# Optimization experiments

Measured on AMD Instinct MI355X. Metric: run time of the kernel, lower is better.

## Reference

```python
import jax, jax.numpy as jnp
import numpy as np

NEG_SLOPE = 0.2  # leaky_relu negative slope (alpha)

def _glorot(key, shape):
    fan_in, fan_out = shape[0], shape[-1]
    lim = jnp.sqrt(6.0 / (fan_in + fan_out))
    return jax.random.uniform(key, shape, jnp.float32, -lim, lim)

def setup_inputs() -> dict:
    key = jax.random.key(0)
    ks = jax.random.split(key, 10)
    N, E, F_IN, HID, HEADS, NCLASS = 50000, 800000, 512, 32, 8, 32
    x = jax.random.normal(ks[0], (N, F_IN), jnp.float32)
    edge_index = jax.random.randint(ks[1], (2, E), 0, N, jnp.int64)
    # layer 1: heads=8, out per head = 32, concat -> 256
    W1 = _glorot(ks[2], (F_IN, HEADS * HID))
    att_src1 = _glorot(ks[3], (HEADS, HID))
    att_dst1 = _glorot(ks[4], (HEADS, HID))
    b1 = jnp.zeros((HEADS * HID,), jnp.float32)
    # layer 2: heads=1, out = nclass
    W2 = _glorot(ks[5], (HEADS * HID, NCLASS))
    att_src2 = _glorot(ks[6], (1, NCLASS))
    att_dst2 = _glorot(ks[7], (1, NCLASS))
    b2 = jnp.zeros((NCLASS,), jnp.float32)
    return {"x": x, "edge_index": edge_index, "W1": W1, "att_src1": att_src1,
            "att_dst1": att_dst1, "b1": b1, "W2": W2, "att_src2": att_src2,
            "att_dst2": att_dst2, "b2": b2}

def gat_conv(x, src, dst, W, a_src, a_dst, bias, num_nodes):
    """PyG GATConv (eval mode, self loops already appended to src/dst)."""
    H, C = a_src.shape
    h = (x @ W).reshape(num_nodes, H, C)                 # [N,H,C]
    score_src = jnp.einsum('nhc,hc->nh', h, a_src)       # [N,H]
    score_dst = jnp.einsum('nhc,hc->nh', h, a_dst)       # [N,H]
    e = jax.nn.leaky_relu(score_src[src] + score_dst[dst], NEG_SLOPE)  # [E,H]
    m = jax.ops.segment_max(e, dst, num_segments=num_nodes)           # [N,H]
    w = jnp.exp(e - m[dst])
    denom = jax.ops.segment_sum(w, dst, num_segments=num_nodes)       # [N,H]
    alpha = w / (denom[dst] + 1e-16)                                  # [E,H]
    out = jax.ops.segment_sum(alpha[:, :, None] * h[src], dst,
                              num_segments=num_nodes)                 # [N,H,C]
    return out.reshape(num_nodes, H * C) + bias

def reference(x, edge_index, W1, att_src1, att_dst1, b1, W2, att_src2, att_dst2, b2):
    N = x.shape[0]
    loops = jnp.arange(N, dtype=edge_index.dtype)
    src = jnp.concatenate([edge_index[0], loops])  # PyG add_self_loops=True
    dst = jnp.concatenate([edge_index[1], loops])
    h = jax.nn.elu(gat_conv(x, src, dst, W1, att_src1, att_dst1, b1, N))
    out = gat_conv(h, src, dst, W2, att_src2, att_dst2, b2, N)
    return out + 1e-06
```

## Files before the change

### kernel.cpp

```cpp
#include <hip/hip_runtime.h>
#include <math.h>

#define N_NODES 50000
#define N_EDGES 800000
#define E2 (N_EDGES + N_NODES)
#define F_IN 512
#define HEADS 8
#define HID 32
#define HC 256
#define NCLASS 32
#define NEG_SLOPE 0.2f

typedef unsigned int uint;
typedef unsigned short ushort;
typedef __attribute__((ext_vector_type(8))) short bf16x8;
typedef __attribute__((ext_vector_type(4))) float f32x4;

#define GLOBAL_LOAD_LDS16(g, l) \
    __builtin_amdgcn_global_load_lds((const __attribute__((address_space(1))) void*)(g), \
                                     (__attribute__((address_space(3))) void*)(l), 16, 0, 0)

__device__ inline uint bf16_rne_bits(float f) {
    uint u = __float_as_uint(f);
    return (u + 0x7fffu + ((u >> 16) & 1u)) >> 16;
}
__device__ inline float bf2f(ushort u) { return __uint_as_float(((uint)u) << 16); }

__global__ void split_w1t_kernel(const float* __restrict__ W1,
                                 ushort* __restrict__ hi, ushort* __restrict__ lo) {
    int t = blockIdx.x * 256 + threadIdx.x;
    int n = t >> 9, k = t & 511;
    float f = W1[k * 256 + n];
    uint h = bf16_rne_bits(f);
    float r = f - __uint_as_float(h << 16);
    hi[t] = (ushort)h;
    lo[t] = (ushort)bf16_rne_bits(r);
}

__global__ void split_w2t_kernel(const float* __restrict__ W2,
                                 ushort* __restrict__ hi, ushort* __restrict__ lo) {
    int t = blockIdx.x * 256 + threadIdx.x;
    int n = t >> 8, k = t & 255;
    float f = W2[k * 32 + n];
    uint h = bf16_rne_bits(f);
    float r = f - __uint_as_float(h << 16);
    hi[t] = (ushort)h;
    lo[t] = (ushort)bf16_rne_bits(r);
}

__global__ void __launch_bounds__(256) gemm1_mfma_kernel(const uint* __restrict__ xp,
        const ushort* __restrict__ bhi, const ushort* __restrict__ blo,
        const float* __restrict__ as1, const float* __restrict__ ad1,
        ushort* __restrict__ C, float* __restrict__ ssrc, float* __restrict__ sdst, int M) {
    __shared__ uint   As[128 * 32];
    __shared__ ushort Bh[128 * 32];
    __shared__ ushort Bl[128 * 32];
    const int tid = threadIdx.x, lane = tid & 63, wave = tid >> 6;
    const int bm = blockIdx.x * 128, bn = blockIdx.y * 128;

    const uint* agp[4]; const uint* alp[4];
    #pragma unroll
    for (int s = 0; s < 4; ++s) {
        int t = wave * 4 + s;
        int p = t * 64 + lane;
        int row = p >> 3, cs = p & 7;
        int c = cs ^ (row & 7);
        int grow = bm + row; if (grow > M - 1) grow = M - 1;
        agp[s] = xp + ((size_t)grow * 512 + c * 4);
        alp[s] = &As[t * 256];
    }
    const ushort* bhgp[2]; const ushort* blgp[2]; const ushort* bhlp[2]; const ushort* bllp[2];
    #pragma unroll
    for (int s = 0; s < 2; ++s) {
        int t = wave * 2 + s;
        int p = t * 64 + lane;
        int row = p >> 2, qs = p & 3;
        int q = qs ^ ((row >> 1) & 3);
        size_t go = (size_t)(bn + row) * 512 + q * 8;
        bhgp[s] = bhi + go; blgp[s] = blo + go;
        bhlp[s] = &Bh[t * 512]; bllp[s] = &Bl[t * 512];
    }

    f32x4 acc[4][4] = {};
    const int wm = (wave >> 1) * 64, wn = (wave & 1) * 64;
    const int fm = lane & 15, quad = lane >> 4;

    for (int kk = 0; kk < 16; ++kk) {
        #pragma unroll
        for (int s = 0; s < 4; ++s) GLOBAL_LOAD_LDS16(agp[s], alp[s]);
        #pragma unroll
        for (int s = 0; s < 2; ++s) {
            GLOBAL_LOAD_LDS16(bhgp[s], bhlp[s]);
            GLOBAL_LOAD_LDS16(blgp[s], bllp[s]);
        }
        #pragma unroll
        for (int s = 0; s < 4; ++s) agp[s] += 32;
        #pragma unroll
        for (int s = 0; s < 2; ++s) { bhgp[s] += 32; blgp[s] += 32; }
        __syncthreads();

        bf16x8 ah[4], al[4], bh[4], bl[4];
        #pragma unroll
        for (int i = 0; i < 4; ++i) {
            int row = wm + i * 16 + fm;
            int sw = row & 7;
            uint4 c0 = *(const uint4*)&As[row * 32 + (((2 * quad)     ^ sw) * 4)];
            uint4 c1 = *(const uint4*)&As[row * 32 + (((2 * quad + 1) ^ sw) * 4)];
            union { uint u[4]; bf16x8 v; } H, L;
            H.u[0] = __builtin_amdgcn_perm(c0.y, c0.x, 0x07060302u);
            H.u[1] = __builtin_amdgcn_perm(c0.w, c0.z, 0x07060302u);
            H.u[2] = __builtin_amdgcn_perm(c1.y, c1.x, 0x07060302u);
            H.u[3] = __builtin_amdgcn_perm(c1.w, c1.z, 0x07060302u);
            uint r0 = __float_as_uint(__uint_as_float(c0.x) - __uint_as_float(c0.x & 0xffff0000u));
            uint r1 = __float_as_uint(__uint_as_float(c0.y) - __uint_as_float(c0.y & 0xffff0000u));
            uint r2 = __float_as_uint(__uint_as_float(c0.z) - __uint_as_float(c0.z & 0xffff0000u));
            uint r3 = __float_as_uint(__uint_as_float(c0.w) - __uint_as_float(c0.w & 0xffff0000u));
            uint r4 = __float_as_uint(__uint_as_float(c1.x) - __uint_as_float(c1.x & 0xffff0000u));
            uint r5 = __float_as_uint(__uint_as_float(c1.y) - __uint_as_float(c1.y & 0xffff0000u));
            uint r6 = __float_as_uint(__uint_as_float(c1.z) - __uint_as_float(c1.z & 0xffff0000u));
            uint r7 = __float_as_uint(__uint_as_float(c1.w) - __uint_as_float(c1.w & 0xffff0000u));
            L.u[0] = __builtin_amdgcn_perm(r1, r0, 0x07060302u);
            L.u[1] = __builtin_amdgcn_perm(r3, r2, 0x07060302u);
            L.u[2] = __builtin_amdgcn_perm(r5, r4, 0x07060302u);
            L.u[3] = __builtin_amdgcn_perm(r7, r6, 0x07060302u);
            ah[i] = H.v; al[i] = L.v;
        }
        #pragma unroll
        for (int j = 0; j < 4; ++j) {
            int row = wn + j * 16 + fm;
            int qs = quad ^ ((row >> 1) & 3);
            bh[j] = *(const bf16x8*)&Bh[row * 32 + qs * 8];
            bl[j] = *(const bf16x8*)&Bl[row * 32 + qs * 8];
        }
        #pragma unroll
        for (int i = 0; i < 4; ++i)
            #pragma unroll
            for (int j = 0; j < 4; ++j) {
                acc[i][j] = __builtin_amdgcn_mfma_f32_16x16x32_bf16(ah[i], bh[j], acc[i][j], 0, 0, 0);
                acc[i][j] = __builtin_amdgcn_mfma_f32_16x16x32_bf16(ah[i], bl[j], acc[i][j], 0, 0, 0);
                acc[i][j] = __builtin_amdgcn_mfma_f32_16x16x32_bf16(al[i], bh[j], acc[i][j], 0, 0, 0);
            }
        __syncthreads();
    }

    #pragma unroll
    for (int i = 0; i < 4; ++i) {
        int rb = bm + wm + i * 16 + quad * 4;
        #pragma unroll
        for (int j = 0; j < 4; ++j) {
            int col = bn + wn + j * 16 + fm;
            #pragma unroll
            for (int r = 0; r < 4; ++r) {
                int row = rb + r;
                if (row < M) C[(size_t)row * 256 + col] = (ushort)bf16_rne_bits(acc[i][j][r]);
            }
        }
    }

    const int head0 = (bn + wn) >> 5;
    const float asA0 = as1[head0 * 32 + fm],      asA1 = as1[head0 * 32 + 16 + fm];
    const float asB0 = as1[head0 * 32 + 32 + fm], asB1 = as1[head0 * 32 + 48 + fm];
    const float adA0 = ad1[head0 * 32 + fm],      adA1 = ad1[head0 * 32 + 16 + fm];
    const float adB0 = ad1[head0 * 32 + 32 + fm], adB1 = ad1[head0 * 32 + 48 + fm];
    #pragma unroll
    for (int i = 0; i < 4; ++i) {
        #pragma unroll
        for (int r = 0; r < 4; ++r) {
            int row = bm + wm + i * 16 + quad * 4 + r;
            float s1A = acc[i][0][r] * asA0 + acc[i][1][r] * asA1;
            float s1B = acc[i][2][r] * asB0 + acc[i][3][r] * asB1;
            float s2A = acc[i][0][r] * adA0 + acc[i][1][r] * adA1;
            float s2B = acc[i][2][r] * adB0 + acc[i][3][r] * adB1;
            #pragma unroll
            for (int off = 1; off < 16; off <<= 1) {
                s1A += __shfl_xor(s1A, off);
                s1B += __shfl_xor(s1B, off);
                s2A += __shfl_xor(s2A, off);
                s2B += __shfl_xor(s2B, off);
            }
            if (fm == 0 && row < M) {
                ssrc[(size_t)row * 8 + head0]     = s1A;
                ssrc[(size_t)row * 8 + head0 + 1] = s1B;
                sdst[(size_t)row * 8 + head0]     = s2A;
                sdst[(size_t)row * 8 + head0 + 1] = s2B;
            }
        }
    }
}

__global__ void __launch_bounds__(256) gemm2_mfma_kernel(const ushort* __restrict__ A,
        const ushort* __restrict__ bh_g, const ushort* __restrict__ bl_g,
        const float* __restrict__ as2, const float* __restrict__ ad2,
        ushort* __restrict__ C, float* __restrict__ ssrc, float* __restrict__ sdst, int M) {
    __shared__ ushort As[128 * 32];
    const int tid = threadIdx.x, lane = tid & 63, wave = tid >> 6;
    const int bm = blockIdx.x * 128;
    const int fm = lane & 15, quad = lane >> 4;
    const int wrow = wave * 32;

    const ushort* agp[2]; const ushort* alp[2];
    #pragma unroll
    for (int s = 0; s < 2; ++s) {
        int t = wave * 2 + s;
        int p = t * 64 + lane;
        int row = p >> 2, qs = p & 3;
        int q = qs ^ ((row >> 1) & 3);
        int gr = bm + row; if (gr > M - 1) gr = M - 1;
        agp[s] = A + (size_t)gr * 256 + q * 8;
        alp[s] = &As[t * 512];
    }

    f32x4 acc[2][2] = {};
    for (int kk = 0; kk < 8; ++kk) {
        GLOBAL_LOAD_LDS16(agp[0], alp[0]);
        GLOBAL_LOAD_LDS16(agp[1], alp[1]);
        agp[0] += 32; agp[1] += 32;
        __syncthreads();
        bf16x8 a[2], bh[2], bl[2];
        #pragma unroll
        for (int i = 0; i < 2; ++i) {
            int row = wrow + i * 16 + fm;
            int q = quad ^ ((row >> 1) & 3);
            a[i] = *(const bf16x8*)&As[row * 32 + q * 8];
        }
        #pragma unroll
        for (int j = 0; j < 2; ++j) {
            size_t off = (size_t)(j * 16 + fm) * 256 + kk * 32 + quad * 8;
            bh[j] = *(const bf16x8*)(bh_g + off);
            bl[j] = *(const bf16x8*)(bl_g + off);
        }
        #pragma unroll
        for (int i = 0; i < 2; ++i)
            #pragma unroll
            for (int j = 0; j < 2; ++j) {
                acc[i][j] = __builtin_amdgcn_mfma_f32_16x16x32_bf16(a[i], bh[j], acc[i][j], 0, 0, 0);
                acc[i][j] = __builtin_amdgcn_mfma_f32_16x16x32_bf16(a[i], bl[j], acc[i][j], 0, 0, 0);
            }
        __syncthreads();
    }

    float a0 = as2[fm], a1 = as2[16 + fm];
    float d0 = ad2[fm], d1 = ad2[16 + fm];
    #pragma unroll
    for (int i = 0; i < 2; ++i) {
        #pragma unroll
        for (int r = 0; r < 4; ++r) {
            int rg = bm + wrow + i * 16 + quad * 4 + r;
            float v0 = acc[i][0][r], v1 = acc[i][1][r];
            float s1 = v0 * a0 + v1 * a1;
            float s2 = v0 * d0 + v1 * d1;
            #pragma unroll
            for (int off = 1; off < 16; off <<= 1) {
                s1 += __shfl_xor(s1, off);
                s2 += __shfl_xor(s2, off);
            }
            if (rg < M) {
                C[(size_t)rg * 32 + fm]      = (ushort)bf16_rne_bits(v0);
                C[(size_t)rg * 32 + 16 + fm] = (ushort)bf16_rne_bits(v1);
                if (fm == 0) { ssrc[rg] = s1; sdst[rg] = s2; }
            }
        }
    }
}

__global__ void count_deg(const int* __restrict__ ei, int* __restrict__ deg) {
    int e = blockIdx.x * blockDim.x + threadIdx.x;
    if (e >= E2) return;
    int dst = (e < N_EDGES) ? ei[N_EDGES + e] : (e - N_EDGES);
    atomicAdd(&deg[dst], 1);
}

#define SCAN_B 256
#define SCAN_NB ((N_NODES + SCAN_B - 1) / SCAN_B)

__global__ void scan1_kernel(const int* __restrict__ deg, int* __restrict__ rowstart,
                             int* __restrict__ blocksum) {
    __shared__ int sm[SCAN_B];
    int t = threadIdx.x, i = blockIdx.x * SCAN_B + t;
    int v = (i < N_NODES) ? deg[i] : 0;
    sm[t] = v; __syncthreads();
    int x = v;
    for (int off = 1; off < SCAN_B; off <<= 1) {
        int y = (t >= off) ? sm[t - off] : 0; __syncthreads();
        x += y; sm[t] = x; __syncthreads();
    }
    if (i <= N_NODES) rowstart[i] = x - v;
    if (t == SCAN_B - 1) blocksum[blockIdx.x] = x;
}

__global__ void scan2_kernel(const int* __restrict__ blocksum, int* __restrict__ blockoff) {
    __shared__ int sm[256];
    int t = threadIdx.x;
    int v = (t < SCAN_NB) ? blocksum[t] : 0;
    sm[t] = v; __syncthreads();
    int x = v;
    for (int off = 1; off < 256; off <<= 1) {
        int y = (t >= off) ? sm[t - off] : 0; __syncthreads();
        x += y; sm[t] = x; __syncthreads();
    }
    if (t < SCAN_NB) blockoff[t] = x - v;
}

__global__ void fill_csr(const int* __restrict__ ei, const int* __restrict__ rowstart,
                         const int* __restrict__ blockoff,
                         int* __restrict__ cursor, int* __restrict__ csr_src) {
    int e = blockIdx.x * blockDim.x + threadIdx.x;
    if (e >= E2) return;
    int src, dst;
    if (e < N_EDGES) { src = ei[e]; dst = ei[N_EDGES + e]; }
    else             { src = e - N_EDGES; dst = src; }
    int p = atomicAdd(&cursor[dst], 1);
    csr_src[rowstart[dst] + blockoff[dst >> 8] + p] = src;
}

__global__ void __launch_bounds__(256) agg1_wave_kernel(const ushort* __restrict__ h,
        const float* __restrict__ ssrc, const float* __restrict__ sdst,
        const int* __restrict__ rowstart, const int* __restrict__ blockoff,
        const int* __restrict__ csr_src,
        const float* __restrict__ bias, ushort* __restrict__ out) {
    const int wid = (blockIdx.x * blockDim.x + threadIdx.x) >> 6;
    if (wid >= N_NODES) return;
    const int lane = threadIdx.x & 63;
    const int hg = lane >> 3;
    const int hl = lane & 7;
    const int n = wid;
    const int beg = rowstart[n] + blockoff[n >> 8];
    const int end = rowstart[n + 1] + blockoff[(n + 1) >> 8];
    const float sdst_n = sdst[(size_t)n * HEADS + hg];

    float4 acc = make_float4(0.f, 0.f, 0.f, 0.f);
    float sw = 0.f;
    const ushort* hc = h + lane * 4;
    const int base = hg << 3;
    for (int e = beg; e < end; e += 8) {
        int ee = e + hl;
        int eidx = ee < end ? ee : end - 1;
        int src_h = csr_src[eidx];
        float sc = ssrc[(size_t)src_h * HEADS + hg] + sdst_n;
        sc = sc > 0.f ? sc : NEG_SLOPE * sc;
        float w_h = (ee < end) ? __expf(sc) : 0.f;
        float wj[8]; int sj[8];
        #pragma unroll
        for (int j = 0; j < 8; ++j) {
            wj[j] = __shfl(w_h, base + j);
            sj[j] = __shfl(src_h, base + j);
        }
        ushort4 v[8];
        #pragma unroll
        for (int j = 0; j < 8; ++j) v[j] = *(const ushort4*)(hc + (size_t)sj[j] * HC);
        #pragma unroll
        for (int j = 0; j < 8; ++j) {
            acc.x += wj[j] * bf2f(v[j].x);
            acc.y += wj[j] * bf2f(v[j].y);
            acc.z += wj[j] * bf2f(v[j].z);
            acc.w += wj[j] * bf2f(v[j].w);
            sw += wj[j];
        }
    }
    float inv = 1.f / (sw + 1e-16f);
    float4 bv = *(const float4*)(bias + lane * 4);
    float4 o;
    o.x = acc.x * inv + bv.x; o.y = acc.y * inv + bv.y;
    o.z = acc.z * inv + bv.z; o.w = acc.w * inv + bv.w;
    o.x = o.x > 0.f ? o.x : expm1f(o.x);
    o.y = o.y > 0.f ? o.y : expm1f(o.y);
    o.z = o.z > 0.f ? o.z : expm1f(o.z);
    o.w = o.w > 0.f ? o.w : expm1f(o.w);
    ushort4 ob;
    ob.x = (ushort)bf16_rne_bits(o.x);
    ob.y = (ushort)bf16_rne_bits(o.y);
    ob.z = (ushort)bf16_rne_bits(o.z);
    ob.w = (ushort)bf16_rne_bits(o.w);
    *(ushort4*)(out + (size_t)n * HC + lane * 4) = ob;
}

__global__ void __launch_bounds__(64) agg2_kernel(const ushort* __restrict__ h2,
        const float* __restrict__ ssrc, const float* __restrict__ sdst,
        const int* __restrict__ rowstart, const int* __restrict__ blockoff,
        const int* __restrict__ csr_src,
        const float* __restrict__ bias, float* __restrict__ out) {
    const int n = blockIdx.x;
    const int beg = rowstart[n] + blockoff[n >> 8];
    const int end = rowstart[n + 1] + blockoff[(n + 1) >> 8];
    const int t = threadIdx.x;
    const float sdst_n = sdst[n];

    const int slot = t >> 4, cp = t & 15;
    float a0 = 0.f, a1 = 0.f, sw = 0.f;
    for (int e = beg + slot; e < end; e += 4) {
        int src = csr_src[e];
        float sc = ssrc[src] + sdst_n;
        sc = sc > 0.f ? sc : NEG_SLOPE * sc;
        float w = __expf(sc);
        uint v = *(const uint*)(h2 + (size_t)src * NCLASS + cp * 2);
        a0 += w * __uint_as_float(v << 16);
        a1 += w * __uint_as_float(v & 0xffff0000u);
        sw += w;
    }
    a0 += __shfl_down(a0, 32); a1 += __shfl_down(a1, 32); sw += __shfl_down(sw, 32);
    a0 += __shfl_down(a0, 16); a1 += __shfl_down(a1, 16); sw += __shfl_down(sw, 16);
    if (t < 16) {
        float inv = 1.f / (sw + 1e-16f);
        float2 o;
        o.x = a0 * inv + bias[cp * 2]     + 1e-6f;
        o.y = a1 * inv + bias[cp * 2 + 1] + 1e-6f;
        *(float2*)(out + (size_t)n * NCLASS + cp * 2) = o;
    }
}

extern "C" void kernel_launch(void* const* d_in, const int* in_sizes, int n_in,
                              void* d_out, int out_size, void* d_ws, size_t ws_size,
                              hipStream_t stream) {
    const float* x        = (const float*)d_in[0];
    const int*   ei       = (const int*)  d_in[1];
    const float* W1       = (const float*)d_in[2];
    const float* att_src1 = (const float*)d_in[3];
    const float* att_dst1 = (const float*)d_in[4];
    const float* b1       = (const float*)d_in[5];
    const float* W2       = (const float*)d_in[6];
    const float* att_src2 = (const float*)d_in[7];
    const float* att_dst2 = (const float*)d_in[8];
    const float* b2       = (const float*)d_in[9];
    float* out = (float*)d_out;

    ushort* w1t_hi = (ushort*)d_ws;
    ushort* w1t_lo = w1t_hi + 256 * 512;
    ushort* w2t_hi = w1t_lo + 256 * 512;
    ushort* w2t_lo = w2t_hi + 32 * 256;
    ushort* h1b    = w2t_lo + 32 * 256;
    ushort* h2b    = h1b + (size_t)N_NODES * HC;
    ushort* out1b  = h2b + (size_t)N_NODES * NCLASS;
    float* ssrc1 = (float*)(out1b + (size_t)N_NODES * HC);
    float* sdst1 = ssrc1 + (size_t)N_NODES * HEADS;
    float* ssrc2 = sdst1 + (size_t)N_NODES * HEADS;
    float* sdst2 = ssrc2 + N_NODES;
    int* rowstart = (int*)(sdst2 + N_NODES);
    int* deg      = rowstart + N_NODES + 1;
    int* cursor   = deg + N_NODES;
    int* csr_src  = cursor + N_NODES;
    int* blocksum = csr_src + E2;
    int* blockoff = blocksum + SCAN_NB;

    hipMemsetAsync(deg, 0, 2 * N_NODES * sizeof(int), stream);
    int eb = (E2 + 255) / 256;
    count_deg<<<eb, 256, 0, stream>>>(ei, deg);
    scan1_kernel<<<SCAN_NB, SCAN_B, 0, stream>>>(deg, rowstart, blocksum);
    scan2_kernel<<<1, 256, 0, stream>>>(blocksum, blockoff);
    fill_csr<<<eb, 256, 0, stream>>>(ei, rowstart, blockoff, cursor, csr_src);

    split_w1t_kernel<<<(256 * 512) / 256, 256, 0, stream>>>(W1, w1t_hi, w1t_lo);
    split_w2t_kernel<<<(32 * 256) / 256, 256, 0, stream>>>(W2, w2t_hi, w2t_lo);

    {
        dim3 grid((N_NODES + 127) / 128, HC / 128);
        gemm1_mfma_kernel<<<grid, 256, 0, stream>>>((const uint*)x, w1t_hi, w1t_lo,
                att_src1, att_dst1, h1b, ssrc1, sdst1, N_NODES);
    }
    agg1_wave_kernel<<<(N_NODES + 3) / 4, 256, 0, stream>>>(h1b, ssrc1, sdst1, rowstart, blockoff, csr_src, b1, out1b);

    gemm2_mfma_kernel<<<(N_NODES + 127) / 128, 256, 0, stream>>>(out1b, w2t_hi, w2t_lo,
            att_src2, att_dst2, h2b, ssrc2, sdst2, N_NODES);
    agg2_kernel<<<N_NODES, 64, 0, stream>>>(h2b, ssrc2, sdst2, rowstart, blockoff, csr_src, b2, out);
}
```

Measured before the change: 404.2 us.

## Double-buffer A tile in LDS and load B fragments directly from global

The GEMM1 kernel now double-buffers the A tile in LDS: it prefetches the next K-slice while computing the current one, which removes one barrier per iteration. The B (weight hi/lo) fragments skip LDS and are read straight from global/L2 into registers, since the weights are small and shared across blocks. This is meant to overlap global loads with MFMA work and cut LDS traffic, at the cost of per-wave uncoalesced global reads of B with exposed latency.

```diff
diff --git a/kernel.cpp b/kernel.cpp
--- a/kernel.cpp
+++ b/kernel.cpp
@@ -52,13 +52,13 @@
         const ushort* __restrict__ bhi, const ushort* __restrict__ blo,
         const float* __restrict__ as1, const float* __restrict__ ad1,
         ushort* __restrict__ C, float* __restrict__ ssrc, float* __restrict__ sdst, int M) {
-    __shared__ uint   As[128 * 32];
-    __shared__ ushort Bh[128 * 32];
-    __shared__ ushort Bl[128 * 32];
+    __shared__ uint As[2][128 * 32];
     const int tid = threadIdx.x, lane = tid & 63, wave = tid >> 6;
     const int bm = blockIdx.x * 128, bn = blockIdx.y * 128;
-
-    const uint* agp[4]; const uint* alp[4];
+    const int fm = lane & 15, quad = lane >> 4;
+    const int wm = (wave >> 1) * 64, wn = (wave & 1) * 64;
+
+    const uint* agp[4]; int alofs[4];
     #pragma unroll
     for (int s = 0; s < 4; ++s) {
         int t = wave * 4 + s;
@@ -67,45 +67,39 @@
         int c = cs ^ (row & 7);
         int grow = bm + row; if (grow > M - 1) grow = M - 1;
         agp[s] = xp + ((size_t)grow * 512 + c * 4);
-        alp[s] = &As[t * 256];
-    }
-    const ushort* bhgp[2]; const ushort* blgp[2]; const ushort* bhlp[2]; const ushort* bllp[2];
-    #pragma unroll
-    for (int s = 0; s < 2; ++s) {
-        int t = wave * 2 + s;
-        int p = t * 64 + lane;
-        int row = p >> 2, qs = p & 3;
-        int q = qs ^ ((row >> 1) & 3);
-        size_t go = (size_t)(bn + row) * 512 + q * 8;
-        bhgp[s] = bhi + go; blgp[s] = blo + go;
-        bhlp[s] = &Bh[t * 512]; bllp[s] = &Bl[t * 512];
-    }
+        alofs[s] = t * 256;
+    }
+    const ushort* bhp = bhi + (size_t)(bn + wn + fm) * 512 + quad * 8;
+    const ushort* blp = blo + (size_t)(bn + wn + fm) * 512 + quad * 8;
 
     f32x4 acc[4][4] = {};
-    const int wm = (wave >> 1) * 64, wn = (wave & 1) * 64;
-    const int fm = lane & 15, quad = lane >> 4;
+
+    #pragma unroll
+    for (int s = 0; s < 4; ++s) { GLOBAL_LOAD_LDS16(agp[s], &As[0][alofs[s]]); agp[s] += 32; }
 
     for (int kk = 0; kk < 16; ++kk) {
-        #pragma unroll
-        for (int s = 0; s < 4; ++s) GLOBAL_LOAD_LDS16(agp[s], alp[s]);
-        #pragma unroll
-        for (int s = 0; s < 2; ++s) {
-            GLOBAL_LOAD_LDS16(bhgp[s], bhlp[s]);
-            GLOBAL_LOAD_LDS16(blgp[s], bllp[s]);
-        }
-        #pragma unroll
-        for (int s = 0; s < 4; ++s) agp[s] += 32;
-        #pragma unroll
-        for (int s = 0; s < 2; ++s) { bhgp[s] += 32; blgp[s] += 32; }
         __syncthreads();
-
-        bf16x8 ah[4], al[4], bh[4], bl[4];
+        const int cur = kk & 1;
+        if (kk < 15) {
+            #pragma unroll
+            for (int s = 0; s < 4; ++s) { GLOBAL_LOAD_LDS16(agp[s], &As[cur ^ 1][alofs[s]]); agp[s] += 32; }
+        }
+
+        bf16x8 bh[4], bl[4];
+        #pragma unroll
+        for (int j = 0; j < 4; ++j) {
+            size_t off = (size_t)j * 16 * 512 + kk * 32;
+            bh[j] = *(const bf16x8*)(bhp + off);
+            bl[j] = *(const bf16x8*)(blp + off);
+        }
+
+        bf16x8 ah[4], al[4];
         #pragma unroll
         for (int i = 0; i < 4; ++i) {
             int row = wm + i * 16 + fm;
             int sw = row & 7;
-            uint4 c0 = *(const uint4*)&As[row * 32 + (((2 * quad)     ^ sw) * 4)];
-            uint4 c1 = *(const uint4*)&As[row * 32 + (((2 * quad + 1) ^ sw) * 4)];
+            uint4 c0 = *(const uint4*)&As[cur][row * 32 + (((2 * quad)     ^ sw) * 4)];
+            uint4 c1 = *(const uint4*)&As[cur][row * 32 + (((2 * quad + 1) ^ sw) * 4)];
             union { uint u[4]; bf16x8 v; } H, L;
             H.u[0] = __builtin_amdgcn_perm(c0.y, c0.x, 0x07060302u);
             H.u[1] = __builtin_amdgcn_perm(c0.w, c0.z, 0x07060302u);
@@ -126,13 +120,6 @@
             ah[i] = H.v; al[i] = L.v;
         }
         #pragma unroll
-        for (int j = 0; j < 4; ++j) {
-            int row = wn + j * 16 + fm;
-            int qs = quad ^ ((row >> 1) & 3);
-            bh[j] = *(const bf16x8*)&Bh[row * 32 + qs * 8];
-            bl[j] = *(const bf16x8*)&Bl[row * 32 + qs * 8];
-        }
-        #pragma unroll
         for (int i = 0; i < 4; ++i)
             #pragma unroll
             for (int j = 0; j < 4; ++j) {
@@ -140,7 +127,6 @@
                 acc[i][j] = __builtin_amdgcn_mfma_f32_16x16x32_bf16(ah[i], bl[j], acc[i][j], 0, 0, 0);
                 acc[i][j] = __builtin_amdgcn_mfma_f32_16x16x32_bf16(al[i], bh[j], acc[i][j], 0, 0, 0);
             }
-        __syncthreads();
     }
 
     #pragma unroll
```

Result: slower. 421.0 us (+4.2%).

## Fuse layer-2 GEMM into layer-1 aggregation and merge prep kernels

Applied to the files above, without the earlier changes.

Layer-1 aggregation now runs 16 nodes per 1024-thread block, keeps the ELU output in shared memory and applies the W2 MFMA plus attention-score reductions in the same kernel. This removes the out1b round trip through global memory and the separate gemm2 launch. The degree count and weight splitting are merged into one prep kernel, and the two-level scan is replaced by a single-block chunked scan, cutting launches. The cost is one large block per 16 nodes, where wave load imbalance and the serial single-block scan may limit throughput.

```diff
diff --git a/kernel.cpp b/kernel.cpp
--- a/kernel.cpp
+++ b/kernel.cpp
@@ -10,6 +10,7 @@
 #define HC 256
 #define NCLASS 32
 #define NEG_SLOPE 0.2f
+#define EB ((E2 + 255) / 256)
 
 typedef unsigned int uint;
 typedef unsigned short ushort;
@@ -26,26 +27,72 @@
 }
 __device__ inline float bf2f(ushort u) { return __uint_as_float(((uint)u) << 16); }
 
-__global__ void split_w1t_kernel(const float* __restrict__ W1,
-                                 ushort* __restrict__ hi, ushort* __restrict__ lo) {
-    int t = blockIdx.x * 256 + threadIdx.x;
-    int n = t >> 9, k = t & 511;
-    float f = W1[k * 256 + n];
-    uint h = bf16_rne_bits(f);
-    float r = f - __uint_as_float(h << 16);
-    hi[t] = (ushort)h;
-    lo[t] = (ushort)bf16_rne_bits(r);
-}
-
-__global__ void split_w2t_kernel(const float* __restrict__ W2,
-                                 ushort* __restrict__ hi, ushort* __restrict__ lo) {
-    int t = blockIdx.x * 256 + threadIdx.x;
-    int n = t >> 8, k = t & 255;
-    float f = W2[k * 32 + n];
-    uint h = bf16_rne_bits(f);
-    float r = f - __uint_as_float(h << 16);
-    hi[t] = (ushort)h;
-    lo[t] = (ushort)bf16_rne_bits(r);
+__global__ void prep_kernel(const int* __restrict__ ei, int* __restrict__ deg,
+                            const float* __restrict__ W1, ushort* __restrict__ w1hi, ushort* __restrict__ w1lo,
+                            const float* __restrict__ W2, ushort* __restrict__ w2hi, ushort* __restrict__ w2lo) {
+    int b = blockIdx.x;
+    if (b < EB) {
+        int e = b * 256 + threadIdx.x;
+        if (e >= E2) return;
+        int dst = (e < N_EDGES) ? ei[N_EDGES + e] : (e - N_EDGES);
+        atomicAdd(&deg[dst], 1);
+    } else if (b < EB + 512) {
+        int t = (b - EB) * 256 + threadIdx.x;
+        int n = t >> 9, k = t & 511;
+        float f = W1[k * 256 + n];
+        uint h = bf16_rne_bits(f);
+        float r = f - __uint_as_float(h << 16);
+        w1hi[t] = (ushort)h;
+        w1lo[t] = (ushort)bf16_rne_bits(r);
+    } else {
+        int t = (b - EB - 512) * 256 + threadIdx.x;
+        int n = t >> 8, k = t & 255;
+        float f = W2[k * 32 + n];
+        uint h = bf16_rne_bits(f);
+        float r = f - __uint_as_float(h << 16);
+        w2hi[t] = (ushort)h;
+        w2lo[t] = (ushort)bf16_rne_bits(r);
+    }
+}
+
+#define SCHUNK 49
+__global__ void __launch_bounds__(1024) scan_all_kernel(const int* __restrict__ deg,
+                                                        int* __restrict__ rowstart) {
+    __shared__ int sm[1024];
+    const int t = threadIdx.x;
+    const int base = t * SCHUNK;
+    int cnt = 50001 - base;
+    if (cnt < 0) cnt = 0;
+    if (cnt > SCHUNK) cnt = SCHUNK;
+
+    int s = 0;
+    for (int i = 0; i < cnt; ++i) {
+        int idx = base + i;
+        if (idx < N_NODES) s += deg[idx];
+    }
+    sm[t] = s; __syncthreads();
+    int x = s;
+    for (int off = 1; off < 1024; off <<= 1) {
+        int y = (t >= off) ? sm[t - off] : 0; __syncthreads();
+        x += y; sm[t] = x; __syncthreads();
+    }
+    int off = x - s;
+    for (int i = 0; i < cnt; ++i) {
+        int idx = base + i;
+        rowstart[idx] = off;
+        if (idx < N_NODES) off += deg[idx];
+    }
+}
+
+__global__ void fill_csr(const int* __restrict__ ei, const int* __restrict__ rowstart,
+                         int* __restrict__ cursor, int* __restrict__ csr_src) {
+    int e = blockIdx.x * blockDim.x + threadIdx.x;
+    if (e >= E2) return;
+    int src, dst;
+    if (e < N_EDGES) { src = ei[e]; dst = ei[N_EDGES + e]; }
+    else             { src = e - N_EDGES; dst = src; }
+    int p = atomicAdd(&cursor[dst], 1);
+    csr_src[rowstart[dst] + p] = src;
 }
 
 __global__ void __launch_bounds__(256) gemm1_mfma_kernel(const uint* __restrict__ xp,
@@ -188,144 +235,21 @@
     }
 }
 
-__global__ void __launch_bounds__(256) gemm2_mfma_kernel(const ushort* __restrict__ A,
-        const ushort* __restrict__ bh_g, const ushort* __restrict__ bl_g,
+__global__ void __launch_bounds__(1024) agg1_fused_kernel(const ushort* __restrict__ h,
+        const float* __restrict__ ssrc, const float* __restrict__ sdst,
+        const int* __restrict__ rowstart, const int* __restrict__ csr_src,
+        const float* __restrict__ bias,
+        const ushort* __restrict__ w2hi, const ushort* __restrict__ w2lo,
         const float* __restrict__ as2, const float* __restrict__ ad2,
-        ushort* __restrict__ C, float* __restrict__ ssrc, float* __restrict__ sdst, int M) {
-    __shared__ ushort As[128 * 32];
-    const int tid = threadIdx.x, lane = tid & 63, wave = tid >> 6;
-    const int bm = blockIdx.x * 128;
-    const int fm = lane & 15, quad = lane >> 4;
-    const int wrow = wave * 32;
-
-    const ushort* agp[2]; const ushort* alp[2];
-    #pragma unroll
-    for (int s = 0; s < 2; ++s) {
-        int t = wave * 2 + s;
-        int p = t * 64 + lane;
-        int row = p >> 2, qs = p & 3;
-        int q = qs ^ ((row >> 1) & 3);
-        int gr = bm + row; if (gr > M - 1) gr = M - 1;
-        agp[s] = A + (size_t)gr * 256 + q * 8;
-        alp[s] = &As[t * 512];
-    }
-
-    f32x4 acc[2][2] = {};
-    for (int kk = 0; kk < 8; ++kk) {
-        GLOBAL_LOAD_LDS16(agp[0], alp[0]);
-        GLOBAL_LOAD_LDS16(agp[1], alp[1]);
-        agp[0] += 32; agp[1] += 32;
-        __syncthreads();
-        bf16x8 a[2], bh[2], bl[2];
-        #pragma unroll
-        for (int i = 0; i < 2; ++i) {
-            int row = wrow + i * 16 + fm;
-            int q = quad ^ ((row >> 1) & 3);
-            a[i] = *(const bf16x8*)&As[row * 32 + q * 8];
-        }
-        #pragma unroll
-        for (int j = 0; j < 2; ++j) {
-            size_t off = (size_t)(j * 16 + fm) * 256 + kk * 32 + quad * 8;
-            bh[j] = *(const bf16x8*)(bh_g + off);
-            bl[j] = *(const bf16x8*)(bl_g + off);
-        }
-        #pragma unroll
-        for (int i = 0; i < 2; ++i)
-            #pragma unroll
-            for (int j = 0; j < 2; ++j) {
-                acc[i][j] = __builtin_amdgcn_mfma_f32_16x16x32_bf16(a[i], bh[j], acc[i][j], 0, 0, 0);
-                acc[i][j] = __builtin_amdgcn_mfma_f32_16x16x32_bf16(a[i], bl[j], acc[i][j], 0, 0, 0);
-            }
-        __syncthreads();
-    }
-
-    float a0 = as2[fm], a1 = as2[16 + fm];
-    float d0 = ad2[fm], d1 = ad2[16 + fm];
-    #pragma unroll
-    for (int i = 0; i < 2; ++i) {
-        #pragma unroll
-        for (int r = 0; r < 4; ++r) {
-            int rg = bm + wrow + i * 16 + quad * 4 + r;
-            float v0 = acc[i][0][r], v1 = acc[i][1][r];
-            float s1 = v0 * a0 + v1 * a1;
-            float s2 = v0 * d0 + v1 * d1;
-            #pragma unroll
-            for (int off = 1; off < 16; off <<= 1) {
-                s1 += __shfl_xor(s1, off);
-                s2 += __shfl_xor(s2, off);
-            }
-            if (rg < M) {
-                C[(size_t)rg * 32 + fm]      = (ushort)bf16_rne_bits(v0);
-                C[(size_t)rg * 32 + 16 + fm] = (ushort)bf16_rne_bits(v1);
-                if (fm == 0) { ssrc[rg] = s1; sdst[rg] = s2; }
-            }
-        }
-    }
-}
-
-__global__ void count_deg(const int* __restrict__ ei, int* __restrict__ deg) {
-    int e = blockIdx.x * blockDim.x + threadIdx.x;
-    if (e >= E2) return;
-    int dst = (e < N_EDGES) ? ei[N_EDGES + e] : (e - N_EDGES);
-    atomicAdd(&deg[dst], 1);
-}
-
-#define SCAN_B 256
-#define SCAN_NB ((N_NODES + SCAN_B - 1) / SCAN_B)
-
-__global__ void scan1_kernel(const int* __restrict__ deg, int* __restrict__ rowstart,
-                             int* __restrict__ blocksum) {
-    __shared__ int sm[SCAN_B];
-    int t = threadIdx.x, i = blockIdx.x * SCAN_B + t;
-    int v = (i < N_NODES) ? deg[i] : 0;
-    sm[t] = v; __syncthreads();
-    int x = v;
-    for (int off = 1; off < SCAN_B; off <<= 1) {
-        int y = (t >= off) ? sm[t - off] : 0; __syncthreads();
-        x += y; sm[t] = x; __syncthreads();
-    }
-    if (i <= N_NODES) rowstart[i] = x - v;
-    if (t == SCAN_B - 1) blocksum[blockIdx.x] = x;
-}
-
-__global__ void scan2_kernel(const int* __restrict__ blocksum, int* __restrict__ blockoff) {
-    __shared__ int sm[256];
-    int t = threadIdx.x;
-    int v = (t < SCAN_NB) ? blocksum[t] : 0;
-    sm[t] = v; __syncthreads();
-    int x = v;
-    for (int off = 1; off < 256; off <<= 1) {
-        int y = (t >= off) ? sm[t - off] : 0; __syncthreads();
-        x += y; sm[t] = x; __syncthreads();
-    }
-    if (t < SCAN_NB) blockoff[t] = x - v;
-}
-
-__global__ void fill_csr(const int* __restrict__ ei, const int* __restrict__ rowstart,
-                         const int* __restrict__ blockoff,
-                         int* __restrict__ cursor, int* __restrict__ csr_src) {
-    int e = blockIdx.x * blockDim.x + threadIdx.x;
-    if (e >= E2) return;
-    int src, dst;
-    if (e < N_EDGES) { src = ei[e]; dst = ei[N_EDGES + e]; }
-    else             { src = e - N_EDGES; dst = src; }
-    int p = atomicAdd(&cursor[dst], 1);
-    csr_src[rowstart[dst] + blockoff[dst >> 8] + p] = src;
-}
-
-__global__ void __launch_bounds__(256) agg1_wave_kernel(const ushort* __restrict__ h,
-        const float* __restrict__ ssrc, const float* __restrict__ sdst,
-        const int* __restrict__ rowstart, const int* __restrict__ blockoff,
-        const int* __restrict__ csr_src,
-        const float* __restrict__ bias, ushort* __restrict__ out) {
-    const int wid = (blockIdx.x * blockDim.x + threadIdx.x) >> 6;
-    if (wid >= N_NODES) return;
-    const int lane = threadIdx.x & 63;
+        ushort* __restrict__ h2b, float* __restrict__ ssrc2, float* __restrict__ sdst2) {
+    __shared__ ushort hsm[16 * 256];
+    __shared__ float scp[2][2][16];
+
+    const int tid = threadIdx.x, lane = tid & 63, wave = tid >> 4 >> 2;
+    const int n = blockIdx.x * 16 + wave;
     const int hg = lane >> 3;
     const int hl = lane & 7;
-    const int n = wid;
-    const int beg = rowstart[n] + blockoff[n >> 8];
-    const int end = rowstart[n + 1] + blockoff[(n + 1) >> 8];
+    const int beg = rowstart[n], end = rowstart[n + 1];
     const float sdst_n = sdst[(size_t)n * HEADS + hg];
 
     float4 acc = make_float4(0.f, 0.f, 0.f, 0.f);
@@ -357,31 +281,68 @@
             sw += wj[j];
         }
     }
-    float inv = 1.f / (sw + 1e-16f);
-    float4 bv = *(const float4*)(bias + lane * 4);
-    float4 o;
-    o.x = acc.x * inv + bv.x; o.y = acc.y * inv + bv.y;
-    o.z = acc.z * inv + bv.z; o.w = acc.w * inv + bv.w;
-    o.x = o.x > 0.f ? o.x : expm1f(o.x);
-    o.y = o.y > 0.f ? o.y : expm1f(o.y);
-    o.z = o.z > 0.f ? o.z : expm1f(o.z);
-    o.w = o.w > 0.f ? o.w : expm1f(o.w);
-    ushort4 ob;
-    ob.x = (ushort)bf16_rne_bits(o.x);
-    ob.y = (ushort)bf16_rne_bits(o.y);
-    ob.z = (ushort)bf16_rne_bits(o.z);
-    ob.w = (ushort)bf16_rne_bits(o.w);
-    *(ushort4*)(out + (size_t)n * HC + lane * 4) = ob;
+    {
+        float inv = 1.f / (sw + 1e-16f);
+        float4 bv = *(const float4*)(bias + lane * 4);
+        float4 o;
+        o.x = acc.x * inv + bv.x; o.y = acc.y * inv + bv.y;
+        o.z = acc.z * inv + bv.z; o.w = acc.w * inv + bv.w;
+        o.x = o.x > 0.f ? o.x : expm1f(o.x);
+        o.y = o.y > 0.f ? o.y : expm1f(o.y);
+        o.z = o.z > 0.f ? o.z : expm1f(o.z);
+        o.w = o.w > 0.f ? o.w : expm1f(o.w);
+        ushort4 ob;
+        ob.x = (ushort)bf16_rne_bits(o.x);
+        ob.y = (ushort)bf16_rne_bits(o.y);
+        ob.z = (ushort)bf16_rne_bits(o.z);
+        ob.w = (ushort)bf16_rne_bits(o.w);
+        *(ushort4*)(&hsm[wave * 256 + lane * 4]) = ob;
+    }
+    __syncthreads();
+
+    if (wave < 2) {
+        const int fm = lane & 15, quad = lane >> 4;
+        const int j = wave;
+        f32x4 a2 = {0.f, 0.f, 0.f, 0.f};
+        #pragma unroll
+        for (int kk = 0; kk < 8; ++kk) {
+            bf16x8 a = *(const bf16x8*)&hsm[fm * 256 + kk * 32 + quad * 8];
+            size_t off = (size_t)(j * 16 + fm) * 256 + kk * 32 + quad * 8;
+            bf16x8 bh = *(const bf16x8*)(w2hi + off);
+            bf16x8 bl = *(const bf16x8*)(w2lo + off);
+            a2 = __builtin_amdgcn_mfma_f32_16x16x32_bf16(a, bh, a2, 0, 0, 0);
+            a2 = __builtin_amdgcn_mfma_f32_16x16x32_bf16(a, bl, a2, 0, 0, 0);
+        }
+        float av = as2[j * 16 + fm], dv = ad2[j * 16 + fm];
+        #pragma unroll
+        for (int r = 0; r < 4; ++r) {
+            int row = quad * 4 + r;
+            int node = blockIdx.x * 16 + row;
+            float v = a2[r];
+            float s1 = v * av, s2 = v * dv;
+            #pragma unroll
+            for (int off = 1; off < 16; off <<= 1) {
+                s1 += __shfl_xor(s1, off);
+                s2 += __shfl_xor(s2, off);
+            }
+            h2b[(size_t)node * 32 + j * 16 + fm] = (ushort)bf16_rne_bits(v);
+            if (fm == 0) { scp[j][0][row] = s1; scp[j][1][row] = s2; }
+        }
+    }
+    __syncthreads();
+    if (wave == 0 && lane < 16) {
+        int node = blockIdx.x * 16 + lane;
+        ssrc2[node] = scp[0][0][lane] + scp[1][0][lane];
+        sdst2[node] = scp[0][1][lane] + scp[1][1][lane];
+    }
 }
 
 __global__ void __launch_bounds__(64) agg2_kernel(const ushort* __restrict__ h2,
         const float* __restrict__ ssrc, const float* __restrict__ sdst,
-        const int* __restrict__ rowstart, const int* __restrict__ blockoff,
-        const int* __restrict__ csr_src,
+        const int* __restrict__ rowstart, const int* __restrict__ csr_src,
         const float* __restrict__ bias, float* __restrict__ out) {
     const int n = blockIdx.x;
-    const int beg = rowstart[n] + blockoff[n >> 8];
-    const int end = rowstart[n + 1] + blockoff[(n + 1) >> 8];
+    const int beg = rowstart[n], end = rowstart[n + 1];
     const int t = threadIdx.x;
     const float sdst_n = sdst[n];
 
@@ -429,8 +390,7 @@
     ushort* w2t_lo = w2t_hi + 32 * 256;
     ushort* h1b    = w2t_lo + 32 * 256;
     ushort* h2b    = h1b + (size_t)N_NODES * HC;
-    ushort* out1b  = h2b + (size_t)N_NODES * NCLASS;
-    float* ssrc1 = (float*)(out1b + (size_t)N_NODES * HC);
+    float* ssrc1 = (float*)(h2b + (size_t)N_NODES * NCLASS);
     float* sdst1 = ssrc1 + (size_t)N_NODES * HEADS;
     float* ssrc2 = sdst1 + (size_t)N_NODES * HEADS;
     float* sdst2 = ssrc2 + N_NODES;
@@ -438,27 +398,17 @@
     int* deg      = rowstart + N_NODES + 1;
     int* cursor   = deg + N_NODES;
     int* csr_src  = cursor + N_NODES;
-    int* blocksum = csr_src + E2;
-    int* blockoff = blocksum + SCAN_NB;
 
     hipMemsetAsync(deg, 0, 2 * N_NODES * sizeof(int), stream);
-    int eb = (E2 + 255) / 256;
-    count_deg<<<eb, 256, 0, stream>>>(ei, deg);
-    scan1_kernel<<<SCAN_NB, SCAN_B, 0, stream>>>(deg, rowstart, blocksum);
-    scan2_kernel<<<1, 256, 0, stream>>>(blocksum, blockoff);
-    fill_csr<<<eb, 256, 0, stream>>>(ei, rowstart, blockoff, cursor, csr_src);
-
-    split_w1t_kernel<<<(256 * 512) / 256, 256, 0, stream>>>(W1, w1t_hi, w1t_lo);
-    split_w2t_kernel<<<(32 * 256) / 256, 256, 0, stream>>>(W2, w2t_hi, w2t_lo);
-
+    prep_kernel<<<EB + 512 + 32, 256, 0, stream>>>(ei, deg, W1, w1t_hi, w1t_lo, W2, w2t_hi, w2t_lo);
+    scan_all_kernel<<<1, 1024, 0, stream>>>(deg, rowstart);
+    fill_csr<<<EB, 256, 0, stream>>>(ei, rowstart, cursor, csr_src);
     {
         dim3 grid((N_NODES + 127) / 128, HC / 128);
         gemm1_mfma_kernel<<<grid, 256, 0, stream>>>((const uint*)x, w1t_hi, w1t_lo,
                 att_src1, att_dst1, h1b, ssrc1, sdst1, N_NODES);
     }
-    agg1_wave_kernel<<<(N_NODES + 3) / 4, 256, 0, stream>>>(h1b, ssrc1, sdst1, rowstart, blockoff, csr_src, b1, out1b);
-
-    gemm2_mfma_kernel<<<(N_NODES + 127) / 128, 256, 0, stream>>>(out1b, w2t_hi, w2t_lo,
-            att_src2, att_dst2, h2b, ssrc2, sdst2, N_NODES);
-    agg2_kernel<<<N_NODES, 64, 0, stream>>>(h2b, ssrc2, sdst2, rowstart, blockoff, csr_src, b2, out);
-}
+    agg1_fused_kernel<<<N_NODES / 16, 1024, 0, stream>>>(h1b, ssrc1, sdst1, rowstart, csr_src,
+            b1, w2t_hi, w2t_lo, att_src2, att_dst2, h2b, ssrc2, sdst2);
+    agg2_kernel<<<N_NODES, 64, 0, stream>>>(h2b, ssrc2, sdst2, rowstart, csr_src, b2, out);
+}
```

Result: slower. 523.7 us (+29.6%).
